# Optimization experiments

Measured on AMD Instinct MI355X. Metric: run time of the kernel, lower is better.

## Reference

```python
import jax, jax.numpy as jnp
import numpy as np

SR = 16000
N_FFT = 400
HOP = 160
N_MELS = 128
F_MIN = 0.0
F_MAX = 8000.0
PCEN_ALPHA = 0.8
PCEN_SMOOTH = 0.04
PCEN_DELTA = 2.0
PCEN_ROOT = 2.0
PCEN_FLOOR = 1e-08
TARGET = (192, 128)


def _hz_to_mel(f):
    return 2595.0 * np.log10(1.0 + f / 700.0)


def _mel_to_hz(m):
    return 700.0 * (10.0 ** (m / 2595.0) - 1.0)


def _mel_filterbank():
    # torchaudio melscale_fbanks, mel_scale='htk', norm=None
    n_freqs = N_FFT // 2 + 1  # 201
    all_freqs = np.linspace(0.0, SR / 2, n_freqs)
    m_pts = np.linspace(_hz_to_mel(F_MIN), _hz_to_mel(F_MAX), N_MELS + 2)
    f_pts = _mel_to_hz(m_pts)
    f_diff = f_pts[1:] - f_pts[:-1]  # (n_mels+1,)
    slopes = f_pts[None, :] - all_freqs[:, None]  # (n_freqs, n_mels+2)
    down = -slopes[:, :-2] / f_diff[:-1]
    up = slopes[:, 2:] / f_diff[1:]
    fb = np.maximum(0.0, np.minimum(down, up))  # (n_freqs, n_mels)
    return jnp.asarray(fb, dtype=jnp.float32)


def _hann_window():
    # periodic hann, matches torch.hann_window(400)
    n = np.arange(N_FFT)
    return jnp.asarray(0.5 * (1.0 - np.cos(2.0 * np.pi * n / N_FFT)), dtype=jnp.float32)


def setup_inputs() -> dict:
    key = jax.random.key(0)
    audio = jax.random.normal(key, (2048, 32000), dtype=jnp.float32)
    return {"audio": audio}


def _mel_spectrogram(audio):
    # center=True reflect pad by n_fft//2
    pad = N_FFT // 2
    x = jnp.pad(audio, ((0, 0), (pad, pad)), mode='reflect')  # (N, 32400)
    T = (x.shape[1] - N_FFT) // HOP + 1  # 201
    idx = jnp.arange(T)[:, None] * HOP + jnp.arange(N_FFT)[None, :]  # (T, n_fft)
    frames = x[:, idx] * _hann_window()  # (N, T, n_fft)
    spec = jnp.fft.rfft(frames, axis=-1)  # (N, T, 201)
    power = jnp.abs(spec) ** 2
    mel = jnp.einsum('ntf,fm->ntm', power, _mel_filterbank())  # (N, T, n_mels)
    return mel


def _pcen(mel_ntm):
    # IIR smoothing over time via scan; mel_ntm: (N, T, M)
    s = PCEN_SMOOTH
    mel_t = jnp.transpose(mel_ntm, (1, 0, 2))  # (T, N, M)

    def step(m_prev, e):
        m_new = (1.0 - s) * m_prev + s * e
        return m_new, m_new

    m0 = mel_t[0]
    _, Ms = jax.lax.scan(step, m0, mel_t[1:])
    M = jnp.concatenate([m0[None], Ms], axis=0)  # (T, N, Mels)
    M = jnp.transpose(M, (1, 0, 2))  # (N, T, Mels)
    inv_r = 1.0 / PCEN_ROOT
    return (mel_ntm / (PCEN_FLOOR + M) ** PCEN_ALPHA + PCEN_DELTA) ** inv_r - PCEN_DELTA ** inv_r


def reference(audio):
    mel = _mel_spectrogram(audio)          # (N, T, 128); original is (N,128,T), PCEN over time either way
    pcen = _pcen(mel)                      # (N, T, 128) == original after transpose(1,2)
    x = pcen[:, None, :, :]                # (N, 1, T, 128)
    N = x.shape[0]
    # bilinear, align_corners=False == jax.image 'linear' (half-pixel centers)
    out = jax.image.resize(x, (N, 1, TARGET[0], TARGET[1]), method='linear')
    return out
```

## Files before the change

kernel.cpp:

```cpp
#include <hip/hip_runtime.h>
#include <math.h>

typedef __attribute__((ext_vector_type(8))) _Float16 half8;
typedef __attribute__((ext_vector_type(4))) float f32x4;
typedef __attribute__((ext_vector_type(4))) unsigned int u32x4;

namespace {
constexpr int NS = 32000, PAD = 200, NT = 201, TOUT = 192, NMEL = 128;
constexpr int PW_STRIDE = 236;
constexpr int BAS_NT = 28;
constexpr int BAS_ELEMS = 13 * 28 * 64 * 8;
constexpr int FB_ELEMS  = 7 * 8 * 64 * 8;
constexpr int OUT_ROW_U16 = TOUT * NMEL * 2;
constexpr int MEL_OFF_U16 = OUT_ROW_U16 - NT * NMEL;
}

__device__ __forceinline__ int swz(int e) { return e ^ (((e >> 7) & 3) << 3); }
__device__ __forceinline__ unsigned short f2h(float f) {
  _Float16 h = (_Float16)f; return __builtin_bit_cast(unsigned short, h);
}
__device__ __forceinline__ float h2f(unsigned short u) {
  return (float)__builtin_bit_cast(_Float16, u);
}

__global__ void setup_tables(unsigned short* __restrict__ ws) {
  int idx = blockIdx.x * 256 + threadIdx.x;
  if (idx < BAS_ELEMS) {
    int j = idx & 7, lane = (idx >> 3) & 63, rest = idx >> 9;
    int nt = rest % BAS_NT, ks = rest / BAS_NT;
    int k   = ks * 32 + ((lane >> 4) << 3) + j;
    int col = nt * 16 + (lane & 15);
    float v = 0.f;
    if (k < 400 && col < 402) {
      int bin = col >> 1;
      int mm  = (k * bin) % 400;
      float th = (float)mm * 0.015707963267948967f;
      float tr = (col & 1) ? sinf(th) : cosf(th);
      float wn = 0.5f * (1.0f - cosf((float)k * 0.015707963267948967f));
      v = wn * tr;
    }
    ws[idx] = f2h(v);
  } else if (idx < BAS_ELEMS + FB_ELEMS) {
    int i2 = idx - BAS_ELEMS;
    int j = i2 & 7, lane = (i2 >> 3) & 63, rest = i2 >> 9;
    int nt = rest % 8, ks = rest / 8;
    int k   = ks * 32 + ((lane >> 4) << 3) + j;
    int mel = nt * 16 + (lane & 15);
    float v = 0.f;
    if (k <= 200) {
      double mhi = 2595.0 * log10(1.0 + 8000.0 / 700.0);
      double ml = mhi * (double)mel / 129.0;
      double mc = mhi * (double)(mel + 1) / 129.0;
      double mr = mhi * (double)(mel + 2) / 129.0;
      double fl = 700.0 * (pow(10.0, ml / 2595.0) - 1.0);
      double fc = 700.0 * (pow(10.0, mc / 2595.0) - 1.0);
      double fr = 700.0 * (pow(10.0, mr / 2595.0) - 1.0);
      double f  = 40.0 * (double)k;
      double wv = fmin((f - fl) / (fc - fl), (fr - f) / (fr - fc));
      v = (float)fmax(0.0, wv);
    }
    ws[idx] = f2h(v);
  }
}

template <int MT>
__global__ __launch_bounds__(256) __attribute__((amdgpu_waves_per_eu(3)))
void dft_mel_kernel(const float* __restrict__ audio, const unsigned short* __restrict__ ws,
                    unsigned short* __restrict__ outu)
{
  constexpr int AU = (MT == 3) ? 7936 : 2816;
  __shared__ unsigned short au[AU];
  __shared__ unsigned short pw16[MT * 16 * PW_STRIDE];
  const int tid = threadIdx.x;
  const int bid = blockIdx.x;
  const int r  = (MT == 3) ? (bid >> 2) : bid;
  const int t0 = (MT == 3) ? ((bid & 3) * 48) : 192;
  const float* __restrict__ ab = audio + (size_t)r * NS;
  const int g0 = t0 * 160 - PAD;

  {
    constexpr int nchunk = AU / 8;
    #pragma unroll 4
    for (int ci = tid; ci < nchunk; ci += 256) {
      half8 hv;
      int gbase = g0 + ci * 8;
      if (gbase >= 0 && gbase + 7 < NS) {
        const float4* p = (const float4*)(ab + gbase);
        float4 x0 = p[0], x1 = p[1];
        hv[0] = (_Float16)x0.x; hv[1] = (_Float16)x0.y;
        hv[2] = (_Float16)x0.z; hv[3] = (_Float16)x0.w;
        hv[4] = (_Float16)x1.x; hv[5] = (_Float16)x1.y;
        hv[6] = (_Float16)x1.z; hv[7] = (_Float16)x1.w;
      } else {
        #pragma unroll
        for (int j = 0; j < 8; ++j) {
          int g = gbase + j;
          if (g < 0) g = -g;
          if (g >= NS) g = 2 * NS - 2 - g;
          hv[j] = (_Float16)ab[g];
        }
      }
      *(half8*)(au + swz(ci * 8)) = hv;
    }
  }
  __syncthreads();

  const int w = tid >> 6, lane = tid & 63, lr = lane & 15, lg = lane >> 4;

  f32x4 acc[MT][7];
  #pragma unroll
  for (int mm = 0; mm < MT; ++mm)
    #pragma unroll
    for (int n = 0; n < 7; ++n) acc[mm][n] = (f32x4){0.f, 0.f, 0.f, 0.f};
  {
    const int laneA = lr * 160 + lg * 8;
    const unsigned short* bptr = ws + ((size_t)(w * 7 * 64 + lane)) * 8;
    for (int ks = 0; ks < 13; ++ks) {
      half8 Bf[7];
      #pragma unroll
      for (int n = 0; n < 7; ++n) Bf[n] = *(const half8*)(bptr + n * 512);
      half8 Af[MT];
      #pragma unroll
      for (int mm = 0; mm < MT; ++mm)
        Af[mm] = *(const half8*)(au + swz(mm * 2560 + ks * 32 + laneA));
      #pragma unroll
      for (int n = 0; n < 7; ++n)
        #pragma unroll
        for (int mm = 0; mm < MT; ++mm)
          acc[mm][n] = __builtin_amdgcn_mfma_f32_16x16x32_f16(Af[mm], Bf[n], acc[mm][n], 0, 0, 0);
      bptr += BAS_NT * 512;
    }
  }
  __syncthreads();

  #pragma unroll
  for (int mm = 0; mm < MT; ++mm) {
    #pragma unroll
    for (int n = 0; n < 7; ++n) {
      int gcol = (w * 7 + n) * 16 + lr;
      int bin  = gcol >> 1;
      float p[4];
      #pragma unroll
      for (int j = 0; j < 4; ++j) {
        float v = acc[mm][n][j];
        int iv = __builtin_bit_cast(int, v);
        float q = __builtin_bit_cast(float,
            __builtin_amdgcn_mov_dpp(iv, 0xB1, 0xF, 0xF, true));
        p[j] = fmaf(v, v, q * q);
      }
      bool odd = (lr & 1);
      int rowb = mm * 16 + lg * 4 + (odd ? 2 : 0);
      pw16[rowb * PW_STRIDE + bin]       = f2h(odd ? p[2] : p[0]);
      pw16[(rowb + 1) * PW_STRIDE + bin] = f2h(odd ? p[3] : p[1]);
    }
  }
  __syncthreads();

  {
    half8 Fb[2][7];
    const unsigned short* fbase = ws + BAS_ELEMS + (size_t)lane * 8;
    #pragma unroll
    for (int nt = 0; nt < 2; ++nt)
      #pragma unroll
      for (int ks = 0; ks < 7; ++ks)
        Fb[nt][ks] = *(const half8*)(fbase + ((size_t)(ks * 8 + 2 * w + nt)) * 512);
    unsigned short* __restrict__ outrow = outu + (size_t)r * OUT_ROW_U16 + MEL_OFF_U16;
    #pragma unroll
    for (int mt = 0; mt < MT; ++mt) {
      half8 Pa[7];
      const unsigned short* psrc = pw16 + (mt * 16 + lr) * PW_STRIDE + lg * 8;
      #pragma unroll
      for (int ks = 0; ks < 7; ++ks) Pa[ks] = *(const half8*)(psrc + ks * 32);
      #pragma unroll
      for (int nt = 0; nt < 2; ++nt) {
        f32x4 a2 = (f32x4){0.f, 0.f, 0.f, 0.f};
        #pragma unroll
        for (int ks = 0; ks < 7; ++ks)
          a2 = __builtin_amdgcn_mfma_f32_16x16x32_f16(Pa[ks], Fb[nt][ks], a2, 0, 0, 0);
        int gm = (2 * w + nt) * 16 + lr;
        #pragma unroll
        for (int j = 0; j < 4; ++j) {
          int t = t0 + mt * 16 + lg * 4 + j;
          if (MT == 3 || t < NT)
            outrow[t * NMEL + gm] = f2h(a2[j]);
        }
      }
    }
  }
}

__global__ __launch_bounds__(1024)
void pcen_resize_kernel(unsigned short* __restrict__ outu)
{
  __shared__ unsigned short mel[NT * 64];
  __shared__ float carry[16][64];
  __shared__ float minb[16][64];
  const int tid = threadIdx.x;
  const int bid = blockIdx.x;
  const int r = bid >> 1, h = bid & 1;
  const unsigned short* src = outu + (size_t)r * OUT_ROW_U16 + MEL_OFF_U16 + h * 64;
  for (int i = tid; i < NT * 8; i += 1024) {
    int t = i >> 3, cc = i & 7;
    *(u32x4*)(mel + t * 64 + cc * 8) = *(const u32x4*)(src + t * 128 + cc * 8);
  }
  __syncthreads();

  const int m = tid & 63, c = tid >> 6;
  const int t0  = (c == 0) ? 0 : (6 + 13 * (c - 1));
  const int len = (c == 0) ? 6 : 13;

  float M = 0.f;
  for (int t = t0; t < t0 + len; ++t) {
    float e = h2f(mel[t * 64 + m]);
    M = (t == 0) ? e : fmaf(0.96f, M, 0.04f * e);
  }
  carry[c][m] = M;
  __syncthreads();
  if (c == 0) {
    float a13 = exp2f(13.0f * log2f(0.96f));
    float acc = carry[0][m];
    minb[1][m] = acc;
    #pragma unroll
    for (int cc = 2; cc < 16; ++cc) {
      acc = fmaf(a13, acc, carry[cc - 1][m]);
      minb[cc][m] = acc;
    }
  }
  __syncthreads();

  float Min = (c == 0) ? 0.f : minb[c][m];
  float wf = 1.f, Mloc = 0.f;
  for (int t = t0; t < t0 + len; ++t) {
    float e = h2f(mel[t * 64 + m]);
    Mloc = (t == 0) ? e : fmaf(0.96f, Mloc, 0.04f * e);
    wf *= 0.96f;
    float Mt = fmaf(wf, Min, Mloc);
    float dn = exp2f(0.8f * log2f(1e-8f + Mt));
    float pc = sqrtf(e / dn + 2.0f) - 1.41421356237309515f;
    mel[t * 64 + m] = f2h(pc);
  }
  __syncthreads();

  float* __restrict__ ob = (float*)outu + (size_t)r * TOUT * NMEL + h * 64;
  const float INVS = 201.0f / 192.0f;
  for (int i = c; i < TOUT; i += 16) {
    float ct = ((float)i + 0.5f) * INVS - 0.5f;
    int jlo = (int)ceilf(ct - INVS);
    int jhi = (int)floorf(ct + INVS);
    if (jlo < 0) jlo = 0;
    if (jhi > NT - 1) jhi = NT - 1;
    float wsum = 0.f, val = 0.f;
    for (int j = jlo; j <= jhi; ++j) {
      float wv = 1.0f - fabsf((float)j - ct) / INVS;
      if (wv > 0.f) { wsum += wv; val = fmaf(wv, h2f(mel[j * 64 + m]), val); }
    }
    ob[(size_t)i * NMEL + m] = val / wsum;
  }
}

extern "C" void kernel_launch(void* const* d_in, const int* in_sizes, int n_in,
                              void* d_out, int out_size, void* d_ws, size_t ws_size,
                              hipStream_t stream) {
  (void)in_sizes; (void)n_in; (void)out_size; (void)ws_size;
  unsigned short* ws = (unsigned short*)d_ws;
  setup_tables<<<(BAS_ELEMS + FB_ELEMS + 255) / 256, 256, 0, stream>>>(ws);
  dft_mel_kernel<3><<<2048 * 4, 256, 0, stream>>>((const float*)d_in[0], ws,
                                                  (unsigned short*)d_out);
  dft_mel_kernel<1><<<2048, 256, 0, stream>>>((const float*)d_in[0], ws,
                                              (unsigned short*)d_out);
  pcen_resize_kernel<<<4096, 1024, 0, stream>>>((unsigned short*)d_out);
}
```

Baseline: 424.0 us.

## Compute real 400-point DFT via even/odd split into two 200-point DFTs

```diff
diff --git a/kernel.cpp b/kernel.cpp
--- a/kernel.cpp
+++ b/kernel.cpp
@@ -8,9 +8,11 @@
 namespace {
 constexpr int NS = 32000, PAD = 200, NT = 201, TOUT = 192, NMEL = 128;
 constexpr int PW_STRIDE = 236;
-constexpr int BAS_NT = 28;
-constexpr int BAS_ELEMS = 13 * 28 * 64 * 8;
-constexpr int FB_ELEMS  = 7 * 8 * 64 * 8;
+constexpr int NT2 = 13;
+constexpr int BAS2_ELEMS = 7 * NT2 * 64 * 8;
+constexpr int WIN_ELEMS  = 448;
+constexpr int FB_OFF     = BAS2_ELEMS + WIN_ELEMS;
+constexpr int FB_ELEMS   = 7 * 8 * 64 * 8;
 constexpr int OUT_ROW_U16 = TOUT * NMEL * 2;
 constexpr int MEL_OFF_U16 = OUT_ROW_U16 - NT * NMEL;
 }
@@ -22,26 +24,37 @@
 __device__ __forceinline__ float h2f(unsigned short u) {
   return (float)__builtin_bit_cast(_Float16, u);
 }
+__device__ __forceinline__ float dppswap(float v) {
+  int iv = __builtin_bit_cast(int, v);
+  return __builtin_bit_cast(float,
+      __builtin_amdgcn_mov_dpp(iv, 0xB1, 0xF, 0xF, true));
+}
 
 __global__ void setup_tables(unsigned short* __restrict__ ws) {
   int idx = blockIdx.x * 256 + threadIdx.x;
-  if (idx < BAS_ELEMS) {
+  if (idx < BAS2_ELEMS) {
     int j = idx & 7, lane = (idx >> 3) & 63, rest = idx >> 9;
-    int nt = rest % BAS_NT, ks = rest / BAS_NT;
-    int k   = ks * 32 + ((lane >> 4) << 3) + j;
+    int nt = rest % NT2, ks = rest / NT2;
+    int n   = ks * 32 + ((lane >> 4) << 3) + j;
     int col = nt * 16 + (lane & 15);
     float v = 0.f;
-    if (k < 400 && col < 402) {
+    if (n < 200 && col < 202) {
       int bin = col >> 1;
-      int mm  = (k * bin) % 400;
-      float th = (float)mm * 0.015707963267948967f;
-      float tr = (col & 1) ? sinf(th) : cosf(th);
-      float wn = 0.5f * (1.0f - cosf((float)k * 0.015707963267948967f));
-      v = wn * tr;
+      int mm  = (bin * n) % 200;
+      float th = (float)mm * 0.03141592653589793f;
+      v = (col & 1) ? sinf(th) : cosf(th);
     }
     ws[idx] = f2h(v);
-  } else if (idx < BAS_ELEMS + FB_ELEMS) {
-    int i2 = idx - BAS_ELEMS;
+  } else if (idx < FB_OFF) {
+    int i2 = idx - BAS2_ELEMS;
+    int j = i2 & 7, lg = (i2 >> 3) & 3, t = i2 >> 5;
+    int ks = t % 7, par = t / 7;
+    int m = ks * 64 + lg * 16 + 2 * j + par;
+    float v = 0.f;
+    if (m < 400) v = 0.5f * (1.0f - cosf((float)m * 0.015707963267948967f));
+    ws[idx] = f2h(v);
+  } else if (idx < FB_OFF + FB_ELEMS) {
+    int i2 = idx - FB_OFF;
     int j = i2 & 7, lane = (i2 >> 3) & 63, rest = i2 >> 9;
     int nt = rest % 8, ks = rest / 8;
     int k   = ks * 32 + ((lane >> 4) << 3) + j;
@@ -64,13 +77,14 @@
 }
 
 template <int MT>
-__global__ __launch_bounds__(256) __attribute__((amdgpu_waves_per_eu(3)))
+__global__ __launch_bounds__(320) __attribute__((amdgpu_waves_per_eu(3)))
 void dft_mel_kernel(const float* __restrict__ audio, const unsigned short* __restrict__ ws,
                     unsigned short* __restrict__ outu)
 {
-  constexpr int AU = (MT == 3) ? 7936 : 2816;
+  constexpr int AU = (MT == 3) ? 7968 : 2848;
   __shared__ unsigned short au[AU];
   __shared__ unsigned short pw16[MT * 16 * PW_STRIDE];
+  __shared__ unsigned short winl[WIN_ELEMS];
   const int tid = threadIdx.x;
   const int bid = blockIdx.x;
   const int r  = (MT == 3) ? (bid >> 2) : bid;
@@ -80,8 +94,7 @@
 
   {
     constexpr int nchunk = AU / 8;
-    #pragma unroll 4
-    for (int ci = tid; ci < nchunk; ci += 256) {
+    for (int ci = tid; ci < nchunk; ci += 320) {
       half8 hv;
       int gbase = g0 + ci * 8;
       if (gbase >= 0 && gbase + 7 < NS) {
@@ -102,90 +115,116 @@
       }
       *(half8*)(au + swz(ci * 8)) = hv;
     }
+    for (int i = tid; i < WIN_ELEMS; i += 320) winl[i] = ws[BAS2_ELEMS + i];
+    for (int i = tid; i < MT * 16 * 24; i += 320) {
+      int row = i / 24, c = 201 + (i % 24);
+      pw16[row * PW_STRIDE + c] = 0;
+    }
   }
   __syncthreads();
 
   const int w = tid >> 6, lane = tid & 63, lr = lane & 15, lg = lane >> 4;
-
-  f32x4 acc[MT][7];
+  const int ntc = (w == 4) ? 1 : 3;
+  const int nt0 = w * 3;
+
+  f32x4 acc_e[MT][3], acc_o[MT][3];
   #pragma unroll
   for (int mm = 0; mm < MT; ++mm)
     #pragma unroll
-    for (int n = 0; n < 7; ++n) acc[mm][n] = (f32x4){0.f, 0.f, 0.f, 0.f};
-  {
-    const int laneA = lr * 160 + lg * 8;
-    const unsigned short* bptr = ws + ((size_t)(w * 7 * 64 + lane)) * 8;
-    for (int ks = 0; ks < 13; ++ks) {
-      half8 Bf[7];
-      #pragma unroll
-      for (int n = 0; n < 7; ++n) Bf[n] = *(const half8*)(bptr + n * 512);
-      half8 Af[MT];
-      #pragma unroll
-      for (int mm = 0; mm < MT; ++mm)
-        Af[mm] = *(const half8*)(au + swz(mm * 2560 + ks * 32 + laneA));
-      #pragma unroll
-      for (int n = 0; n < 7; ++n)
-        #pragma unroll
-        for (int mm = 0; mm < MT; ++mm)
-          acc[mm][n] = __builtin_amdgcn_mfma_f32_16x16x32_f16(Af[mm], Bf[n], acc[mm][n], 0, 0, 0);
-      bptr += BAS_NT * 512;
-    }
-  }
-  __syncthreads();
-
-  #pragma unroll
-  for (int mm = 0; mm < MT; ++mm) {
-    #pragma unroll
-    for (int n = 0; n < 7; ++n) {
-      int gcol = (w * 7 + n) * 16 + lr;
-      int bin  = gcol >> 1;
-      float p[4];
+    for (int n = 0; n < 3; ++n) {
+      acc_e[mm][n] = (f32x4){0.f, 0.f, 0.f, 0.f};
+      acc_o[mm][n] = (f32x4){0.f, 0.f, 0.f, 0.f};
+    }
+  for (int ks = 0; ks < 7; ++ks) {
+    half8 Bf[3];
+    #pragma unroll
+    for (int n = 0; n < 3; ++n)
+      if (n < ntc)
+        Bf[n] = *(const half8*)(ws + ((size_t)((ks * NT2 + nt0 + n) * 64 + lane)) * 8);
+    half8 We = *(const half8*)(winl + ((0 * 7 + ks) * 4 + lg) * 8);
+    half8 Wo = *(const half8*)(winl + ((1 * 7 + ks) * 4 + lg) * 8);
+    #pragma unroll
+    for (int mm = 0; mm < MT; ++mm) {
+      int base = mm * 2560 + lr * 160 + ks * 64 + lg * 16;
+      half8 r0 = *(const half8*)(au + swz(base));
+      half8 r1 = *(const half8*)(au + swz(base + 8));
+      half8 ae, ao;
       #pragma unroll
       for (int j = 0; j < 4; ++j) {
-        float v = acc[mm][n][j];
-        int iv = __builtin_bit_cast(int, v);
-        float q = __builtin_bit_cast(float,
-            __builtin_amdgcn_mov_dpp(iv, 0xB1, 0xF, 0xF, true));
-        p[j] = fmaf(v, v, q * q);
+        ae[j] = r0[2 * j];     ao[j] = r0[2 * j + 1];
+        ae[j + 4] = r1[2 * j]; ao[j + 4] = r1[2 * j + 1];
       }
+      ae = ae * We;
+      ao = ao * Wo;
+      #pragma unroll
+      for (int n = 0; n < 3; ++n)
+        if (n < ntc) {
+          acc_e[mm][n] = __builtin_amdgcn_mfma_f32_16x16x32_f16(ae, Bf[n], acc_e[mm][n], 0, 0, 0);
+          acc_o[mm][n] = __builtin_amdgcn_mfma_f32_16x16x32_f16(ao, Bf[n], acc_o[mm][n], 0, 0, 0);
+        }
+    }
+  }
+  __syncthreads();
+
+  #pragma unroll
+  for (int n = 0; n < 3; ++n)
+    if (n < ntc) {
+      int kp = (nt0 + n) * 8 + (lr >> 1);
+      float th = (float)kp * 0.015707963267948967f;
+      float cth = cosf(th), sth = sinf(th);
       bool odd = (lr & 1);
-      int rowb = mm * 16 + lg * 4 + (odd ? 2 : 0);
-      pw16[rowb * PW_STRIDE + bin]       = f2h(odd ? p[2] : p[0]);
-      pw16[(rowb + 1) * PW_STRIDE + bin] = f2h(odd ? p[3] : p[1]);
-    }
-  }
+      #pragma unroll
+      for (int mm = 0; mm < MT; ++mm) {
+        #pragma unroll
+        for (int j = 0; j < 4; ++j) {
+          float ev = acc_e[mm][n][j], ov = acc_o[mm][n][j];
+          float ep = dppswap(ev),     op = dppswap(ov);
+          float ec = odd ? ep : ev,   es = odd ? ev : ep;
+          float oc = odd ? op : ov,   os = odd ? ov : op;
+          float u  = cth * oc - sth * os;
+          float v2 = cth * os + sth * oc;
+          float a  = odd ? (ec - u)  : (ec + u);
+          float b  = odd ? (es - v2) : (es + v2);
+          float p  = a * a + b * b;
+          if (kp <= 100) {
+            int bin = odd ? (200 - kp) : kp;
+            int row = mm * 16 + lg * 4 + j;
+            pw16[row * PW_STRIDE + bin] = f2h(p);
+          }
+        }
+      }
+    }
   __syncthreads();
 
   {
-    half8 Fb[2][7];
-    const unsigned short* fbase = ws + BAS_ELEMS + (size_t)lane * 8;
-    #pragma unroll
-    for (int nt = 0; nt < 2; ++nt)
-      #pragma unroll
-      for (int ks = 0; ks < 7; ++ks)
-        Fb[nt][ks] = *(const half8*)(fbase + ((size_t)(ks * 8 + 2 * w + nt)) * 512);
+    const int fcnt = (w < 3) ? 2 : 1;
+    const int f0   = (w < 3) ? 2 * w : 6 + (w - 3);
     unsigned short* __restrict__ outrow = outu + (size_t)r * OUT_ROW_U16 + MEL_OFF_U16;
     #pragma unroll
-    for (int mt = 0; mt < MT; ++mt) {
-      half8 Pa[7];
-      const unsigned short* psrc = pw16 + (mt * 16 + lr) * PW_STRIDE + lg * 8;
-      #pragma unroll
-      for (int ks = 0; ks < 7; ++ks) Pa[ks] = *(const half8*)(psrc + ks * 32);
-      #pragma unroll
-      for (int nt = 0; nt < 2; ++nt) {
-        f32x4 a2 = (f32x4){0.f, 0.f, 0.f, 0.f};
+    for (int ff = 0; ff < 2; ++ff)
+      if (ff < fcnt) {
+        int fbnt = f0 + ff;
+        half8 Fb[7];
         #pragma unroll
         for (int ks = 0; ks < 7; ++ks)
-          a2 = __builtin_amdgcn_mfma_f32_16x16x32_f16(Pa[ks], Fb[nt][ks], a2, 0, 0, 0);
-        int gm = (2 * w + nt) * 16 + lr;
+          Fb[ks] = *(const half8*)(ws + FB_OFF + ((size_t)((ks * 8 + fbnt) * 64 + lane)) * 8);
+        int gm = fbnt * 16 + lr;
         #pragma unroll
-        for (int j = 0; j < 4; ++j) {
-          int t = t0 + mt * 16 + lg * 4 + j;
-          if (MT == 3 || t < NT)
-            outrow[t * NMEL + gm] = f2h(a2[j]);
+        for (int mt = 0; mt < MT; ++mt) {
+          const unsigned short* psrc = pw16 + (mt * 16 + lr) * PW_STRIDE + lg * 8;
+          f32x4 a2 = (f32x4){0.f, 0.f, 0.f, 0.f};
+          #pragma unroll
+          for (int ks = 0; ks < 7; ++ks)
+            a2 = __builtin_amdgcn_mfma_f32_16x16x32_f16(*(const half8*)(psrc + ks * 32),
+                                                        Fb[ks], a2, 0, 0, 0);
+          #pragma unroll
+          for (int j = 0; j < 4; ++j) {
+            int t = t0 + mt * 16 + lg * 4 + j;
+            if (MT == 3 || t < NT)
+              outrow[t * NMEL + gm] = f2h(a2[j]);
+          }
         }
       }
-    }
   }
 }
 
@@ -263,10 +302,11 @@
                               hipStream_t stream) {
   (void)in_sizes; (void)n_in; (void)out_size; (void)ws_size;
   unsigned short* ws = (unsigned short*)d_ws;
-  setup_tables<<<(BAS_ELEMS + FB_ELEMS + 255) / 256, 256, 0, stream>>>(ws);
-  dft_mel_kernel<3><<<2048 * 4, 256, 0, stream>>>((const float*)d_in[0], ws,
+  const int total = FB_OFF + FB_ELEMS;
+  setup_tables<<<(total + 255) / 256, 256, 0, stream>>>(ws);
+  dft_mel_kernel<3><<<2048 * 4, 320, 0, stream>>>((const float*)d_in[0], ws,
                                                   (unsigned short*)d_out);
-  dft_mel_kernel<1><<<2048, 256, 0, stream>>>((const float*)d_in[0], ws,
+  dft_mel_kernel<1><<<2048, 320, 0, stream>>>((const float*)d_in[0], ws,
                                               (unsigned short*)d_out);
   pcen_resize_kernel<<<4096, 1024, 0, stream>>>((unsigned short*)d_out);
 }
```

After: 517.2 us. 22.0% more time.
